# Optimization experiments

Hardware: AMD Instinct MI355X
Metric: run time of the kernel (lower is better)

The kernel has to match this reference:

```python
import jax, jax.numpy as jnp
import numpy as np

DN = ('NCHW', 'OIHW', 'NCHW')

def _conv(x, w, stride, pad, groups=1):
    return jax.lax.conv_general_dilated(x, w, (stride, stride), pad,
                                        feature_group_count=groups,
                                        dimension_numbers=DN)

def _bn(x, s, b):
    # eval-mode BatchNorm folded to per-channel affine
    return x * s[:, None, None] + b[:, None, None]

def _gelu(x):
    return jax.nn.gelu(x, approximate=False)  # torch nn.GELU default = exact erf

def _region_dw(x, dw_w, s1, b1, pw_w, s2, b2, g):
    # Vectorized RegionLayerDW: split [B,C,H,W] into g*g tiles, apply per-tile
    # depthwise3x3 -> BN -> GELU -> 1x1 -> BN -> +residual, reassemble.
    B, C, H, W = x.shape
    th, tw = H // g, W // g
    t = x.reshape(B, C, g, th, g, tw).transpose(2, 4, 0, 1, 3, 5)
    t = t.reshape(g * g, B, C, th, tw)  # [G,B,C,th,tw]
    def tile(xt, w, ts1, tb1, pw, ts2, tb2):
        h = _conv(xt, w, 1, ((1, 1), (1, 1)), groups=C)  # depthwise 3x3
        h = _gelu(_bn(h, ts1, tb1))
        h = jnp.einsum('bchw,oc->bohw', h, pw)  # 1x1 conv
        return _bn(h, ts2, tb2) + xt
    y = jax.vmap(tile)(t, dw_w, s1, b1, pw_w, s2, b2)
    y = y.reshape(g, g, B, C, th, tw).transpose(2, 3, 0, 4, 1, 5)
    return y.reshape(B, C, H, W)

def _forward(x, r1_w, r1_s, r1_b, r1_dw, r1_s1, r1_b1, r1_pw, r1_s2, r1_b2,
             r2_w, r2_s, r2_b, r2_dw, r2_s1, r2_b1, r2_pw, r2_s2, r2_b2,
             h1_w1, h1_s1, h1_b1, h1_w2, h1_s2, h1_b2, h1_w3, h1_s3, h1_b3,
             h2_w1, h2_s1, h2_b1, h2_w2, h2_s2, h2_b2,
             h3_w, h3_s, h3_b):
    B = x.shape[0]
    # region1: 5x5 conv 3->24, BN, GELU, RegionLayerDW grid 7x7; then outer GELU
    r1 = _gelu(_bn(_conv(x, r1_w, 1, ((2, 2), (2, 2))), r1_s, r1_b))
    r1 = _region_dw(r1, r1_dw, r1_s1, r1_b1, r1_pw, r1_s2, r1_b2, 7)
    region1 = _gelu(r1)
    # region2: 3x3 conv 24->48, BN, GELU, RegionLayerDW grid 4x4; outer GELU
    r2 = _gelu(_bn(_conv(region1, r2_w, 1, ((1, 1), (1, 1))), r2_s, r2_b))
    r2 = _region_dw(r2, r2_dw, r2_s1, r2_b1, r2_pw, r2_s2, r2_b2, 4)
    region2 = _gelu(r2)
    # hMLP branch1: 3 -> 48(k4s4) -> 48(k2s2) -> 256(k2s2)
    h = _gelu(_bn(_conv(x, h1_w1, 4, 'VALID'), h1_s1, h1_b1))
    h = _gelu(_bn(_conv(h, h1_w2, 2, 'VALID'), h1_s2, h1_b2))
    branch1 = _bn(_conv(h, h1_w3, 2, 'VALID'), h1_s3, h1_b3)
    # hMLP branch2: 24 -> 48(k4s4) -> 256(k4s4)
    g2 = _gelu(_bn(_conv(region1, h2_w1, 4, 'VALID'), h2_s1, h2_b1))
    branch2 = _bn(_conv(g2, h2_w2, 4, 'VALID'), h2_s2, h2_b2)
    # hMLP branch3: 48 -> 256(k16s16)
    branch3 = _bn(_conv(region2, h3_w, 16, 'VALID'), h3_s, h3_b)
    out = jnp.concatenate((branch1, branch2, branch3), axis=1)  # [B,768,14,14]
    return jnp.transpose(out.reshape(B, out.shape[1], -1), (0, 2, 1))  # [B,196,768]


def setup_inputs() -> dict:
    key = jax.random.key(0)
    ks = [key]
    def nk():
        ks[0], k = jax.random.split(ks[0])
        return k
    def rn(shape, scale=0.05):
        return jax.random.normal(nk(), shape, jnp.float32) * scale
    def sc(shape):
        return 1.0 + rn(shape)
    B = 16
    d = {}
    d['x'] = rn((B, 3, 224, 224), 1.0)
    d['r1_w'] = rn((24, 3, 5, 5)); d['r1_s'] = sc((24,)); d['r1_b'] = rn((24,))
    d['r1_dw'] = rn((49, 24, 1, 3, 3)); d['r1_s1'] = sc((49, 24)); d['r1_b1'] = rn((49, 24))
    d['r1_pw'] = rn((49, 24, 24)); d['r1_s2'] = sc((49, 24)); d['r1_b2'] = rn((49, 24))
    d['r2_w'] = rn((48, 24, 3, 3)); d['r2_s'] = sc((48,)); d['r2_b'] = rn((48,))
    d['r2_dw'] = rn((16, 48, 1, 3, 3)); d['r2_s1'] = sc((16, 48)); d['r2_b1'] = rn((16, 48))
    d['r2_pw'] = rn((16, 48, 48)); d['r2_s2'] = sc((16, 48)); d['r2_b2'] = rn((16, 48))
    d['h1_w1'] = rn((48, 3, 4, 4)); d['h1_s1'] = sc((48,)); d['h1_b1'] = rn((48,))
    d['h1_w2'] = rn((48, 48, 2, 2)); d['h1_s2'] = sc((48,)); d['h1_b2'] = rn((48,))
    d['h1_w3'] = rn((256, 48, 2, 2)); d['h1_s3'] = sc((256,)); d['h1_b3'] = rn((256,))
    d['h2_w1'] = rn((48, 24, 4, 4)); d['h2_s1'] = sc((48,)); d['h2_b1'] = rn((48,))
    d['h2_w2'] = rn((256, 48, 4, 4)); d['h2_s2'] = sc((256,)); d['h2_b2'] = rn((256,))
    d['h3_w'] = rn((256, 48, 16, 16)); d['h3_s'] = sc((256,)); d['h3_b'] = rn((256,))
    return d


def reference(x, r1_w, r1_s, r1_b, r1_dw, r1_s1, r1_b1, r1_pw, r1_s2, r1_b2,
              r2_w, r2_s, r2_b, r2_dw, r2_s1, r2_b1, r2_pw, r2_s2, r2_b2,
              h1_w1, h1_s1, h1_b1, h1_w2, h1_s2, h1_b2, h1_w3, h1_s3, h1_b3,
              h2_w1, h2_s1, h2_b1, h2_w2, h2_s2, h2_b2,
              h3_w, h3_s, h3_b):
    return _forward(x, r1_w, r1_s, r1_b, r1_dw, r1_s1, r1_b1, r1_pw, r1_s2, r1_b2,
                    r2_w, r2_s, r2_b, r2_dw, r2_s1, r2_b1, r2_pw, r2_s2, r2_b2,
                    h1_w1, h1_s1, h1_b1, h1_w2, h1_s2, h1_b2, h1_w3, h1_s3, h1_b3,
                    h2_w1, h2_s1, h2_b1, h2_w2, h2_s2, h2_b2,
                    h3_w, h3_s, h3_b)
```

## Files before the change

kernel.cpp:

```cpp
#include <hip/hip_runtime.h>
#include <hip/hip_bf16.h>
#include <math.h>

typedef __attribute__((ext_vector_type(8))) short short8;
typedef __attribute__((ext_vector_type(4))) float f32x4;

__device__ __forceinline__ float gelu_f(float x) {
  float ax = fabsf(x);
  float z = ax * 0.70710678118654752f;
  float t = __builtin_amdgcn_rcpf(1.0f + 0.3275911f * z);
  float p = t * (0.254829592f +
           t * (-0.284496736f +
           t * (1.421413741f +
           t * (-1.453152027f + t * 1.061405429f))));
  float e = __expf(-z * z);
  float erf_abs = 1.0f - p * e;
  return 0.5f * x + 0.5f * ax * erf_abs;
}

template<bool TBL, bool GELU, bool TOOUT>
__global__ __launch_bounds__(256) void convgemm_k(
    const float* __restrict__ in, const float* __restrict__ w,
    const float* __restrict__ bns, const float* __restrict__ bnb,
    float* __restrict__ out,
    int Cin, int H, int W, int ks, int stride, int pad, int ls,
    int OH, int OW, int N, int K, int ch0) {
  __shared__ __align__(16) float sA[16][64];
  __shared__ __align__(16) float sB[16][64];
  __shared__ int sTbl[256];
  const int tid = threadIdx.x;
  if (TBL) {
    int kk2 = ks * ks;
    for (int k = tid; k < K; k += 256) {
      int ic = k / kk2, r = k - ic * kk2;
      sTbl[k] = (ic << 16) | ((r / ks) << 8) | (r % ks);
    }
  }
  const int m0 = blockIdx.x * 64, n0 = blockIdx.y * 64;
  const int mm = tid >> 2, kq = tid & 3;
  const int OHW = OH * OW, HW = H * W;
  int m = m0 + mm;
  int bI = m / OHW; int r = m - bI * OHW;
  int oh = r / OW;  int ow = r - oh * OW;
  const int ihBase = oh * stride - pad, iwBase = ow * stride - pad;
  const int inBase = bI * Cin * HW;
  const int tm = tid & 15, tn = tid >> 4;
  float acc[4][4] = {};
  for (int k0 = 0; k0 < K; k0 += 16) {
    __syncthreads();
#pragma unroll
    for (int i = 0; i < 4; ++i) {
      int kk = kq * 4 + i, k = k0 + kk;
      float v = 0.0f;
      if (k < K) {
        int ic, dy, dx;
        if (TBL) {
          int tv = sTbl[k]; ic = tv >> 16; dy = (tv >> 8) & 255; dx = tv & 255;
        } else {
          ic = k >> (2 * ls);
          int r2 = k & ((1 << (2 * ls)) - 1);
          dy = r2 >> ls; dx = r2 & ((1 << ls) - 1);
        }
        int ih = ihBase + dy, iw = iwBase + dx;
        if (ih >= 0 && ih < H && iw >= 0 && iw < W)
          v = in[inBase + ic * HW + ih * W + iw];
      }
      sA[kk][mm] = v;
    }
#pragma unroll
    for (int i = 0; i < 4; ++i) {
      int kk = kq * 4 + i, k = k0 + kk;
      int n = n0 + mm;
      float v = 0.0f;
      if (n < N && k < K) v = w[n * K + k];
      sB[kk][mm] = v;
    }
    __syncthreads();
#pragma unroll
    for (int kk = 0; kk < 16; ++kk) {
      float4 a4 = *(const float4*)&sA[kk][tm * 4];
      float4 b4 = *(const float4*)&sB[kk][tn * 4];
      acc[0][0] += a4.x * b4.x; acc[0][1] += a4.x * b4.y;
      acc[0][2] += a4.x * b4.z; acc[0][3] += a4.x * b4.w;
      acc[1][0] += a4.y * b4.x; acc[1][1] += a4.y * b4.y;
      acc[1][2] += a4.y * b4.z; acc[1][3] += a4.y * b4.w;
      acc[2][0] += a4.z * b4.x; acc[2][1] += a4.z * b4.y;
      acc[2][2] += a4.z * b4.z; acc[2][3] += a4.z * b4.w;
      acc[3][0] += a4.w * b4.x; acc[3][1] += a4.w * b4.y;
      acc[3][2] += a4.w * b4.z; acc[3][3] += a4.w * b4.w;
    }
  }
#pragma unroll
  for (int i = 0; i < 4; ++i) {
    int mI = m0 + tm * 4 + i;
    int bO = mI / OHW; int rr = mI - bO * OHW;
#pragma unroll
    for (int j = 0; j < 4; ++j) {
      int n = n0 + tn * 4 + j;
      if (n < N) {
        float v = acc[i][j] * bns[n] + bnb[n];
        if (GELU) v = gelu_f(v);
        if (TOOUT) {
          out[(bO * OHW + rr) * 768 + ch0 + n] = v;
        } else {
          int oh2 = rr / OW, ow2 = rr - oh2 * OW;
          out[((bO * N + n) * OH + oh2) * OW + ow2] = v;
        }
      }
    }
  }
}

template<int CIN, int KS, int STRIDE, int PAD, int NN, int KP, bool GELU,
         int OUTMODE, int NVALID = NN>
__global__ __launch_bounds__(256) void nhwc_conv_mfma(
    const __hip_bfloat16* __restrict__ in, const __hip_bfloat16* __restrict__ wb,
    const float* __restrict__ bns, const float* __restrict__ bnb,
    float* __restrict__ out, int Hin, int Win, int OW, int OHW) {
  constexpr int K = KS * KS * CIN;
  constexpr int LROW = KP + 8;
  __shared__ __align__(16) __hip_bfloat16 sA[64][LROW];
  __shared__ __align__(16) __hip_bfloat16 sB[NN][LROW];
  const int tid = threadIdx.x;
  const float4 f4z = make_float4(0.f, 0.f, 0.f, 0.f);
  if constexpr (CIN == 4) {
    const int m = tid & 63, tg = tid >> 6;
    const int mg = blockIdx.x * 64 + m;
    const int bI = mg / OHW; int pix = mg - bI * OHW;
    const int oh = pix / OW, ow = pix - oh * OW;
    for (int dy = tg; dy < KS; dy += 4) {
      const int ih = oh * STRIDE - PAD + dy;
      __hip_bfloat16* dst = &sA[m][dy * KS * 4];
#pragma unroll
      for (int j = 0; j < KS; ++j) {
        int iw = ow * STRIDE - PAD + j;
        uint2 v = make_uint2(0u, 0u);
        if (ih >= 0 && ih < Hin && iw >= 0 && iw < Win)
          v = *(const uint2*)(in + (((size_t)bI * Hin + ih) * Win + iw) * 4);
        *(uint2*)(dst + j * 4) = v;
      }
    }
    if (tg == 3) {
      for (int c = K; c < KP; c += 4) *(uint2*)&sA[m][c] = make_uint2(0u, 0u);
    }
  } else {
    const int m = tid & 63, dy = tid >> 6;
    const int mg = blockIdx.x * 64 + m;
    const int bI = mg / OHW; int pix = mg - bI * OHW;
    const int oh = pix / OW, ow = pix - oh * OW;
    if (dy < KS) {
      const int ih = oh * STRIDE - PAD + dy;
      __hip_bfloat16* dst = &sA[m][dy * KS * CIN];
      if (ih < 0 || ih >= Hin) {
#pragma unroll
        for (int i = 0; i < KS * CIN / 8; ++i) ((float4*)dst)[i] = f4z;
      } else {
        const __hip_bfloat16* srow = in + ((size_t)bI * Hin + ih) * Win * CIN;
#pragma unroll
        for (int j = 0; j < KS; ++j) {
          int iw = ow * STRIDE - PAD + j;
          if (PAD > 0 && (iw < 0 || iw >= Win)) {
#pragma unroll
            for (int i = 0; i < CIN / 8; ++i) ((float4*)(dst + j * CIN))[i] = f4z;
          } else {
            const float4* s4 = (const float4*)(srow + (size_t)iw * CIN);
#pragma unroll
            for (int i = 0; i < CIN / 8; ++i) ((float4*)(dst + j * CIN))[i] = s4[i];
          }
        }
      }
    } else if (K < KP) {
#pragma unroll
      for (int c = K; c < KP + 8; c += 8) *(float4*)&sA[m][c] = f4z;
    }
  }
  {
    constexpr int NV = NN * KP / 8;
    const float4* w4 = (const float4*)wb;
    for (int i = tid; i < NV; i += 256) {
      int n = i / (KP / 8), c = i - n * (KP / 8);
      *(float4*)&sB[n][c * 8] = w4[i];
    }
  }
  __syncthreads();
  constexpr int NT = NN / 16;
  const int wave = tid >> 6, lane = tid & 63;
  const int fm = lane & 15, quad = lane >> 4;
  const int wm = wave * 16;
  f32x4 acc[NT] = {};
#pragma unroll
  for (int ks = 0; ks < KP / 32; ++ks) {
    short8 a = *(const short8*)&sA[wm + fm][ks * 32 + quad * 8];
#pragma unroll
    for (int j = 0; j < NT; ++j) {
      short8 b = *(const short8*)&sB[j * 16 + fm][ks * 32 + quad * 8];
      acc[j] = __builtin_amdgcn_mfma_f32_16x16x32_bf16(a, b, acc[j], 0, 0, 0);
    }
  }
  const int mg0 = blockIdx.x * 64 + wm + quad * 4;
  const int bI = mg0 / OHW, pix = mg0 - bI * OHW;
#pragma unroll
  for (int j = 0; j < NT; ++j) {
    int n = j * 16 + fm;
    if (n >= NVALID) continue;
    float s = bns[n], bb = bnb[n];
    float v[4];
#pragma unroll
    for (int e = 0; e < 4; ++e) {
      v[e] = acc[j][e] * s + bb;
      if (GELU) v[e] = gelu_f(v[e]);
    }
    if (OUTMODE == 0) {
      float4 v4 = make_float4(v[0], v[1], v[2], v[3]);
      *(float4*)&out[((size_t)(bI * NVALID + n)) * OHW + pix] = v4;
    } else {
      __hip_bfloat16* ob = (__hip_bfloat16*)out;
#pragma unroll
      for (int e = 0; e < 4; ++e)
        ob[((size_t)(bI * OHW + pix + e)) * NVALID + n] = (__hip_bfloat16)v[e];
    }
  }
}

__global__ __launch_bounds__(256, 4) void region2_mfma(
    const __hip_bfloat16* __restrict__ in, const float* __restrict__ dww,
    const float* __restrict__ s1v, const float* __restrict__ b1v,
    const __hip_bfloat16* __restrict__ pwb,
    const float* __restrict__ s2v, const float* __restrict__ b2v,
    __hip_bfloat16* __restrict__ out) {
  __shared__ __align__(16) __hip_bfloat16 sIn[10][10][56];
  __shared__ __align__(16) __hip_bfloat16 sH[64][64];
  __shared__ __align__(16) __hip_bfloat16 sW[48][64];
  __shared__ float sDW[48][9];
  __shared__ float sS1[48], sB1[48], sS2[48], sB2[48];
  const int t = blockIdx.x, sb = blockIdx.y, b = blockIdx.z;
  const int gy = t >> 2, gx = t & 3;
  const int py0 = (sb / 7) * 8, px0 = (sb % 7) * 8;
  const int Y0 = gy * 56, X0 = gx * 56;
  const int tid = threadIdx.x;
  for (int i = tid; i < 48 * 8; i += 256) {
    int n = i >> 3, g = i & 7;
    float4 v = *(const float4*)&pwb[(size_t)(t * 48 + n) * 64 + g * 8];
    *(float4*)&sW[n][((g ^ (n & 7)) * 8)] = v;
  }
  for (int i = tid; i < 432; i += 256) ((float*)sDW)[i] = dww[t * 432 + i];
  if (tid < 48) {
    sS1[tid] = s1v[t * 48 + tid]; sB1[tid] = b1v[t * 48 + tid];
    sS2[tid] = s2v[t * 48 + tid]; sB2[tid] = b2v[t * 48 + tid];
  }
  for (int i = tid; i < 600; i += 256) {
    int px = i / 6, grp = i - px * 6;
    int r = px / 10, c = px - r * 10;
    int ly = py0 + r - 1, lx = px0 + c - 1;
    uint4 v = make_uint4(0u, 0u, 0u, 0u);
    if (ly >= 0 && ly < 56 && lx >= 0 && lx < 56)
      v = *(const uint4*)(in + (((size_t)b * 224 + Y0 + ly) * 224 + X0 + lx) * 48 +
                          grp * 8);
    *(uint4*)&sIn[r][c][grp * 8] = v;
  }
  __syncthreads();
  if (tid < 192) {
    const int cg = tid >> 4;
    const int rem = tid & 15;
    const int col = rem >> 1;
    const int rh = rem & 1;
    const int ch0 = cg * 4;
    float wv[4][9], s14[4], b14[4];
#pragma unroll
    for (int c4 = 0; c4 < 4; ++c4) {
#pragma unroll
      for (int q = 0; q < 9; ++q) wv[c4][q] = sDW[ch0 + c4][q];
      s14[c4] = sS1[ch0 + c4]; b14[c4] = sB1[ch0 + c4];
    }
    float win[3][12];
#pragma unroll
    for (int rr = 0; rr < 6; ++rr) {
      int r = rh * 4 + rr;
      float* wr = win[rr % 3];
#pragma unroll
      for (int cc = 0; cc < 3; ++cc) {
        uint2 u = *(const uint2*)&sIn[r][col + cc][ch0];
        wr[cc * 4 + 0] = __uint_as_float(u.x << 16);
        wr[cc * 4 + 1] = __uint_as_float(u.x & 0xffff0000u);
        wr[cc * 4 + 2] = __uint_as_float(u.y << 16);
        wr[cc * 4 + 3] = __uint_as_float(u.y & 0xffff0000u);
      }
      if (rr >= 2) {
        const float* ra = win[(rr - 2) % 3];
        const float* rb = win[(rr - 1) % 3];
        const float* rc = win[rr % 3];
        int px = (rh * 4 + rr - 2) * 8 + col;
        __hip_bfloat16 hv[4];
#pragma unroll
        for (int c4 = 0; c4 < 4; ++c4) {
          float a = ra[c4] * wv[c4][0] + ra[4 + c4] * wv[c4][1] + ra[8 + c4] * wv[c4][2]
                  + rb[c4] * wv[c4][3] + rb[4 + c4] * wv[c4][4] + rb[8 + c4] * wv[c4][5]
                  + rc[c4] * wv[c4][6] + rc[4 + c4] * wv[c4][7] + rc[8 + c4] * wv[c4][8];
          hv[c4] = (__hip_bfloat16)gelu_f(a * s14[c4] + b14[c4]);
        }
        *(uint2*)&sH[px][((cg >> 1) ^ (px & 7)) * 8 + (cg & 1) * 4] = *(uint2*)hv;
      }
    }
  } else {
    for (int i = tid - 192; i < 128; i += 64) {
      int px = i >> 1, g = 6 + (i & 1);
      *(float4*)&sH[px][(g ^ (px & 7)) * 8] = make_float4(0.f, 0.f, 0.f, 0.f);
    }
  }
  __syncthreads();
  const int wave = tid >> 6, lane = tid & 63;
  const int fm = lane & 15, quad = lane >> 4;
  const int px = wave * 16 + fm, pxk = px & 7;
  f32x4 acc[3] = {};
#pragma unroll
  for (int ks = 0; ks < 2; ++ks) {
    short8 hb = *(const short8*)&sH[px][((ks * 4 + quad) ^ pxk) * 8];
#pragma unroll
    for (int m = 0; m < 3; ++m) {
      int wr = m * 16 + fm;
      short8 wa = *(const short8*)&sW[wr][((ks * 4 + quad) ^ (wr & 7)) * 8];
      acc[m] = __builtin_amdgcn_mfma_f32_16x16x32_bf16(wa, hb, acc[m], 0, 0, 0);
    }
  }
  const int row = px >> 3, col = px & 7;
  __hip_bfloat16* obase =
      out + (((size_t)b * 224 + Y0 + py0 + row) * 224 + X0 + px0 + col) * 48;
#pragma unroll
  for (int m = 0; m < 3; ++m) {
    int ch0m = m * 16 + quad * 4;
    uint2 ru = *(const uint2*)&sIn[row + 1][col + 1][ch0m];
    float res[4];
    res[0] = __uint_as_float(ru.x << 16);
    res[1] = __uint_as_float(ru.x & 0xffff0000u);
    res[2] = __uint_as_float(ru.y << 16);
    res[3] = __uint_as_float(ru.y & 0xffff0000u);
    __hip_bfloat16 vb[4];
#pragma unroll
    for (int e = 0; e < 4; ++e) {
      int ch = ch0m + e;
      float v = acc[m][e] * sS2[ch] + sB2[ch] + res[e];
      vb[e] = (__hip_bfloat16)gelu_f(v);
    }
    *(uint2*)&obase[ch0m] = *(uint2*)vb;
  }
}

__global__ __launch_bounds__(256, 4) void region1_mfma(
    const __hip_bfloat16* __restrict__ in, const float* __restrict__ dww,
    const float* __restrict__ s1v, const float* __restrict__ b1v,
    const __hip_bfloat16* __restrict__ pwb,
    const float* __restrict__ s2v, const float* __restrict__ b2v,
    __hip_bfloat16* __restrict__ out) {
  __shared__ __align__(16) __hip_bfloat16 sIn[10][10][24];
  __shared__ __align__(16) __hip_bfloat16 sH[64][32];
  __shared__ __align__(16) __hip_bfloat16 sW[32][32];
  __shared__ float sDW[24][9];
  __shared__ float sS1[24], sB1[24], sS2[24], sB2[24];
  const int t = blockIdx.x, sb = blockIdx.y, b = blockIdx.z;
  const int gy = t / 7, gx = t % 7;
  const int py0 = (sb >> 2) * 8, px0 = (sb & 3) * 8;
  const int Y0 = gy * 32, X0 = gx * 32;
  const int tid = threadIdx.x;
  for (int i = tid; i < 128; i += 256) {
    int n = i >> 2, g = i & 3;
    float4 v = make_float4(0.f, 0.f, 0.f, 0.f);
    if (n < 24) v = *(const float4*)&pwb[(size_t)(t * 24 + n) * 32 + g * 8];
    *(float4*)&sW[n][(g ^ (n & 3)) * 8] = v;
  }
  for (int i = tid; i < 216; i += 256) ((float*)sDW)[i] = dww[t * 216 + i];
  if (tid < 24) {
    sS1[tid] = s1v[t * 24 + tid]; sB1[tid] = b1v[t * 24 + tid];
    sS2[tid] = s2v[t * 24 + tid]; sB2[tid] = b2v[t * 24 + tid];
  }
  for (int i = tid; i < 300; i += 256) {
    int px = i / 3, grp = i - px * 3;
    int r = px / 10, c = px - r * 10;
    int ly = py0 + r - 1, lx = px0 + c - 1;
    uint4 v = make_uint4(0u, 0u, 0u, 0u);
    if (ly >= 0 && ly < 32 && lx >= 0 && lx < 32)
      v = *(const uint4*)(in + (((size_t)b * 224 + Y0 + ly) * 224 + X0 + lx) * 24 +
                          grp * 8);
    *(uint4*)&sIn[r][c][grp * 8] = v;
  }
  __syncthreads();
  if (tid < 192) {
    const int cg = tid >> 5;
    const int rem = tid & 31;
    const int col = rem >> 2;
    const int rq = rem & 3;
    const int ch0 = cg * 4;
    float wv[4][9], s14[4], b14[4];
#pragma unroll
    for (int c4 = 0; c4 < 4; ++c4) {
#pragma unroll
      for (int q = 0; q < 9; ++q) wv[c4][q] = sDW[ch0 + c4][q];
      s14[c4] = sS1[ch0 + c4]; b14[c4] = sB1[ch0 + c4];
    }
    float win[3][12];
#pragma unroll
    for (int rr = 0; rr < 4; ++rr) {
      int r = rq * 2 + rr;
      float* wr = win[rr % 3];
#pragma unroll
      for (int cc = 0; cc < 3; ++cc) {
        uint2 u = *(const uint2*)&sIn[r][col + cc][ch0];
        wr[cc * 4 + 0] = __uint_as_float(u.x << 16);
        wr[cc * 4 + 1] = __uint_as_float(u.x & 0xffff0000u);
        wr[cc * 4 + 2] = __uint_as_float(u.y << 16);
        wr[cc * 4 + 3] = __uint_as_float(u.y & 0xffff0000u);
      }
      if (rr >= 2) {
        const float* ra = win[(rr - 2) % 3];
        const float* rb = win[(rr - 1) % 3];
        const float* rc = win[rr % 3];
        int px = (rq * 2 + rr - 2) * 8 + col;
        __hip_bfloat16 hv[4];
#pragma unroll
        for (int c4 = 0; c4 < 4; ++c4) {
          float a = ra[c4] * wv[c4][0] + ra[4 + c4] * wv[c4][1] + ra[8 + c4] * wv[c4][2]
                  + rb[c4] * wv[c4][3] + rb[4 + c4] * wv[c4][4] + rb[8 + c4] * wv[c4][5]
                  + rc[c4] * wv[c4][6] + rc[4 + c4] * wv[c4][7] + rc[8 + c4] * wv[c4][8];
          hv[c4] = (__hip_bfloat16)gelu_f(a * s14[c4] + b14[c4]);
        }
        *(uint2*)&sH[px][((cg >> 1) ^ (px & 3)) * 8 + (cg & 1) * 4] = *(uint2*)hv;
      }
    }
  } else {
    int px = tid - 192;
    *(float4*)&sH[px][(3 ^ (px & 3)) * 8] = make_float4(0.f, 0.f, 0.f, 0.f);
  }
  __syncthreads();
  const int wave = tid >> 6, lane = tid & 63;
  const int fm = lane & 15, quad = lane >> 4;
  const int px = wave * 16 + fm;
  short8 hb = *(const short8*)&sH[px][(quad ^ (px & 3)) * 8];
  f32x4 acc[2] = {};
#pragma unroll
  for (int m = 0; m < 2; ++m) {
    int wr = m * 16 + fm;
    short8 wa = *(const short8*)&sW[wr][(quad ^ (wr & 3)) * 8];
    acc[m] = __builtin_amdgcn_mfma_f32_16x16x32_bf16(wa, hb, acc[m], 0, 0, 0);
  }
  const int row = px >> 3, col = px & 7;
  __hip_bfloat16* obase =
      out + (((size_t)b * 224 + Y0 + py0 + row) * 224 + X0 + px0 + col) * 24;
#pragma unroll
  for (int m = 0; m < 2; ++m) {
    int ch0m = m * 16 + quad * 4;
    if (ch0m < 24) {
      uint2 ru = *(const uint2*)&sIn[row + 1][col + 1][ch0m];
      float res[4];
      res[0] = __uint_as_float(ru.x << 16);
      res[1] = __uint_as_float(ru.x & 0xffff0000u);
      res[2] = __uint_as_float(ru.y << 16);
      res[3] = __uint_as_float(ru.y & 0xffff0000u);
      __hip_bfloat16 vb[4];
#pragma unroll
      for (int e = 0; e < 4; ++e) {
        int ch = ch0m + e;
        float v = acc[m][e] * sS2[ch] + sB2[ch] + res[e];
        vb[e] = (__hip_bfloat16)gelu_f(v);
      }
      *(uint2*)&obase[ch0m] = *(uint2*)vb;
    }
  }
}

template<int PS, int IMGW, int KTOT, int KSL, bool ATOMIC>
__global__ __launch_bounds__(256) void patch_gemm_mfma(
    const __hip_bfloat16* __restrict__ A, const __hip_bfloat16* __restrict__ Wb,
    const float* __restrict__ scale, const float* __restrict__ bias,
    float* __restrict__ out, int M, int ch0) {
  constexpr int RUN = PS * 48;
  __shared__ __align__(16) __hip_bfloat16 sA[64][64];
  __shared__ __align__(16) __hip_bfloat16 sB[64][64];
  const int tid = threadIdx.x;
  const int m0 = blockIdx.x * 64, n0 = blockIdx.y * 64;
  const int kBase = blockIdx.z * KSL;
  const int mi = tid >> 2, seg = tid & 3;
  int m = m0 + mi; int mc = (m < M) ? m : (M - 1);
  int bI = mc / 196; int r = mc - bI * 196;
  int oh = r / 14, ow = r - oh * 14;
  const __hip_bfloat16* Abase =
      A + (((size_t)bI * IMGW + oh * PS) * IMGW + ow * PS) * 48;
  const __hip_bfloat16* Wrow = Wb + (size_t)(n0 + mi) * KTOT;
  const int wave = tid >> 6, lane = tid & 63;
  const int wm = (wave & 1) * 32, wn = (wave >> 1) * 32;
  const int fm = lane & 15, quad = lane >> 4;
  const int sw = fm & 7;
  f32x4 acc[2][2] = {};
  for (int k0 = kBase; k0 < kBase + KSL; k0 += 64) {
    int dy = k0 / RUN, rem = k0 - dy * RUN;
    __syncthreads();
    {
      const __hip_bfloat16* p = Abase + (size_t)dy * IMGW * 48 + rem + seg * 16;
      float4 v0 = *(const float4*)p;
      float4 v1 = *(const float4*)(p + 8);
      int key = mi & 7;
      *(float4*)&sA[mi][((seg * 2) ^ key) * 8] = v0;
      *(float4*)&sA[mi][((seg * 2 + 1) ^ key) * 8] = v1;
      const __hip_bfloat16* q = Wrow + k0 + seg * 16;
      float4 w0 = *(const float4*)q;
      float4 w1 = *(const float4*)(q + 8);
      *(float4*)&sB[mi][((seg * 2) ^ key) * 8] = w0;
      *(float4*)&sB[mi][((seg * 2 + 1) ^ key) * 8] = w1;
    }
    __syncthreads();
#pragma unroll
    for (int ks = 0; ks < 2; ++ks) {
      int cg = (ks * 4 + quad) ^ sw;
#pragma unroll
      for (int i = 0; i < 2; ++i) {
        short8 a = *(const short8*)&sA[wm + i * 16 + fm][cg * 8];
#pragma unroll
        for (int j = 0; j < 2; ++j) {
          short8 b = *(const short8*)&sB[wn + j * 16 + fm][cg * 8];
          acc[i][j] = __builtin_amdgcn_mfma_f32_16x16x32_bf16(a, b, acc[i][j], 0, 0, 0);
        }
      }
    }
  }
#pragma unroll
  for (int i = 0; i < 2; ++i) {
#pragma unroll
    for (int j = 0; j < 2; ++j) {
      int gn = n0 + wn + j * 16 + fm;
      float sc = scale[gn];
#pragma unroll
      for (int e = 0; e < 4; ++e) {
        int gm = m0 + wm + i * 16 + quad * 4 + e;
        if (gm < M) {
          if (ATOMIC)
            atomicAdd(&out[(size_t)gm * 768 + ch0 + gn], acc[i][j][e] * sc);
          else
            out[(size_t)gm * 768 + ch0 + gn] = acc[i][j][e] * sc + bias[gn];
        }
      }
    }
  }
}

__global__ void init_b3(float* __restrict__ out, const float* __restrict__ bias) {
  int i = blockIdx.x * 256 + threadIdx.x;
  if (i < 16 * 196 * 256) {
    int n = i & 255, bp = i >> 8;
    out[bp * 768 + 512 + n] = bias[n];
  }
}

__global__ void reorder_w_k(const float* __restrict__ w, __hip_bfloat16* __restrict__ o,
                            int N, int Cin, int ks, int KP) {
  int i = blockIdx.x * 256 + threadIdx.x;
  if (i >= N * KP) return;
  int n = i / KP, k = i - n * KP;
  float v = 0.f;
  int K = ks * ks * Cin;
  if (k < K) {
    int dy = k / (ks * Cin); int r = k - dy * ks * Cin;
    int dx = r / Cin, ic = r - dx * Cin;
    v = w[((n * Cin + ic) * ks + dy) * ks + dx];
  }
  o[i] = (__hip_bfloat16)v;
}

__global__ void reorder_w4(const float* __restrict__ w, __hip_bfloat16* __restrict__ o,
                           int Nout, int Nreal, int Cp, int Cr, int ks, int KP) {
  int i = blockIdx.x * 256 + threadIdx.x;
  if (i >= Nout * KP) return;
  int n = i / KP, k = i - n * KP;
  float v = 0.f;
  if (n < Nreal && k < ks * ks * Cp) {
    int dy = k / (ks * Cp); int r = k - dy * ks * Cp;
    int dx = r / Cp, ic = r - dx * Cp;
    if (ic < Cr) v = w[((n * Cr + ic) * ks + dy) * ks + dx];
  }
  o[i] = (__hip_bfloat16)v;
}

__global__ void rw_pw(const float* __restrict__ pw, __hip_bfloat16* __restrict__ o) {
  int i = blockIdx.x * 256 + threadIdx.x;
  if (i >= 16 * 48 * 64) return;
  int t = i / 3072, r = i - t * 3072;
  int n = r >> 6, k = r & 63;
  float v = (k < 48) ? pw[(t * 48 + n) * 48 + k] : 0.f;
  o[i] = (__hip_bfloat16)v;
}

__global__ void rw_pw1(const float* __restrict__ pw, __hip_bfloat16* __restrict__ o) {
  int i = blockIdx.x * 256 + threadIdx.x;
  if (i >= 49 * 24 * 32) return;
  int t = i / 768, r = i - t * 768;
  int n = r >> 5, k = r & 31;
  float v = (k < 24) ? pw[(t * 24 + n) * 24 + k] : 0.f;
  o[i] = (__hip_bfloat16)v;
}

__global__ void xcvt(const float* __restrict__ x, __hip_bfloat16* __restrict__ o) {
  int i = blockIdx.x * 256 + threadIdx.x;
  if (i >= 802816) return;
  int b = i / 50176, p = i - b * 50176;
  const float* src = x + (size_t)b * 150528 + p;
  __hip_bfloat16 v[4];
  v[0] = (__hip_bfloat16)src[0];
  v[1] = (__hip_bfloat16)src[50176];
  v[2] = (__hip_bfloat16)src[100352];
  v[3] = (__hip_bfloat16)0.0f;
  *(uint2*)&o[(size_t)i * 4] = *(uint2*)v;
}

extern "C" void kernel_launch(void* const* d_in, const int* in_sizes, int n_in,
                              void* d_out, int out_size, void* d_ws, size_t ws_size,
                              hipStream_t stream) {
  const float* x     = (const float*)d_in[0];
  const float* r1_w  = (const float*)d_in[1];
  const float* r1_s  = (const float*)d_in[2];
  const float* r1_b  = (const float*)d_in[3];
  const float* r1_dw = (const float*)d_in[4];
  const float* r1_s1 = (const float*)d_in[5];
  const float* r1_b1 = (const float*)d_in[6];
  const float* r1_pw = (const float*)d_in[7];
  const float* r1_s2 = (const float*)d_in[8];
  const float* r1_b2 = (const float*)d_in[9];
  const float* r2_w  = (const float*)d_in[10];
  const float* r2_s  = (const float*)d_in[11];
  const float* r2_b  = (const float*)d_in[12];
  const float* r2_dw = (const float*)d_in[13];
  const float* r2_s1 = (const float*)d_in[14];
  const float* r2_b1 = (const float*)d_in[15];
  const float* r2_pw = (const float*)d_in[16];
  const float* r2_s2 = (const float*)d_in[17];
  const float* r2_b2 = (const float*)d_in[18];
  const float* h1_w1 = (const float*)d_in[19];
  const float* h1_s1 = (const float*)d_in[20];
  const float* h1_b1 = (const float*)d_in[21];
  const float* h1_w2 = (const float*)d_in[22];
  const float* h1_s2 = (const float*)d_in[23];
  const float* h1_b2 = (const float*)d_in[24];
  const float* h1_w3 = (const float*)d_in[25];
  const float* h1_s3 = (const float*)d_in[26];
  const float* h1_b3 = (const float*)d_in[27];
  const float* h2_w1 = (const float*)d_in[28];
  const float* h2_s1 = (const float*)d_in[29];
  const float* h2_b1 = (const float*)d_in[30];
  const float* h2_w2 = (const float*)d_in[31];
  const float* h2_s2 = (const float*)d_in[32];
  const float* h2_b2 = (const float*)d_in[33];
  const float* h3_w  = (const float*)d_in[34];
  const float* h3_s  = (const float*)d_in[35];
  const float* h3_b  = (const float*)d_in[36];
  float* out = (float*)d_out;

  float* F = (float*)d_ws;
  __hip_bfloat16* R1b   = (__hip_bfloat16*)F;
  __hip_bfloat16* C5b   = (__hip_bfloat16*)(F + 9633792);
  __hip_bfloat16* T1b   = (__hip_bfloat16*)(F + 9633792);
  __hip_bfloat16* T2b   = (__hip_bfloat16*)(F + 28901376);
  __hip_bfloat16* h3wb  = (__hip_bfloat16*)(F + 48168960);
  __hip_bfloat16* r2wb  = (__hip_bfloat16*)(F + 49741824);
  __hip_bfloat16* h2w1b = (__hip_bfloat16*)(F + 49747200);
  __hip_bfloat16* pw2wb = (__hip_bfloat16*)(F + 49756416);
  __hip_bfloat16* r1wb  = (__hip_bfloat16*)(F + 49780992);
  __hip_bfloat16* h2w2b = (__hip_bfloat16*)(F + 49783040);
  __hip_bfloat16* xb    = (__hip_bfloat16*)(F + 49881344);
  __hip_bfloat16* S1b   = (__hip_bfloat16*)(F + 51486976);
  float* S1             = F + 52691200;
  float* S2             = F + 55099648;
  __hip_bfloat16* pw1wb = (__hip_bfloat16*)(F + 55701760);

  dim3 blk(256);

  xcvt<<<dim3(3136), blk, 0, stream>>>(x, xb);
  reorder_w_k<<<dim3(12288), blk, 0, stream>>>(h3_w, h3wb, 256, 48, 16, 12288);
  reorder_w_k<<<dim3(42), blk, 0, stream>>>(r2_w, r2wb, 48, 24, 3, 224);
  reorder_w_k<<<dim3(72), blk, 0, stream>>>(h2_w1, h2w1b, 48, 24, 4, 384);
  reorder_w_k<<<dim3(768), blk, 0, stream>>>(h2_w2, h2w2b, 256, 48, 4, 768);
  reorder_w4<<<dim3(16), blk, 0, stream>>>(r1_w, r1wb, 32, 24, 4, 3, 5, 128);
  rw_pw<<<dim3(192), blk, 0, stream>>>(r2_pw, pw2wb);
  rw_pw1<<<dim3(147), blk, 0, stream>>>(r1_pw, pw1wb);

  nhwc_conv_mfma<4, 5, 1, 2, 32, 128, true, 1, 24><<<dim3(12544), blk, 0, stream>>>(
      xb, r1wb, r1_s, r1_b, (float*)C5b, 224, 224, 224, 50176);
  region1_mfma<<<dim3(49, 16, 16), blk, 0, stream>>>(
      C5b, r1_dw, r1_s1, r1_b1, pw1wb, r1_s2, r1_b2, R1b);
  nhwc_conv_mfma<24, 4, 4, 0, 48, 384, true, 1><<<dim3(784), blk, 0, stream>>>(
      R1b, h2w1b, h2_s1, h2_b1, (float*)S1b, 224, 224, 56, 3136);
  patch_gemm_mfma<4, 56, 768, 768, false><<<dim3(49, 4, 1), blk, 0, stream>>>(
      S1b, h2w2b, h2_s2, h2_b2, out, 3136, 256);
  convgemm_k<false, true, false><<<dim3(784, 1), blk, 0, stream>>>(
      x, h1_w1, h1_s1, h1_b1, S1, 3, 224, 224, 4, 4, 0, 2, 56, 56, 48, 48, 0);
  convgemm_k<false, true, false><<<dim3(196, 1), blk, 0, stream>>>(
      S1, h1_w2, h1_s2, h1_b2, S2, 48, 56, 56, 2, 2, 0, 1, 28, 28, 48, 192, 0);
  convgemm_k<false, false, true><<<dim3(49, 4), blk, 0, stream>>>(
      S2, h1_w3, h1_s3, h1_b3, out, 48, 28, 28, 2, 2, 0, 1, 14, 14, 256, 192, 0);
  init_b3<<<dim3(3136), blk, 0, stream>>>(out, h3_b);
  nhwc_conv_mfma<24, 3, 1, 1, 48, 224, true, 1><<<dim3(12544), blk, 0, stream>>>(
      R1b, r2wb, r2_s, r2_b, (float*)T1b, 224, 224, 224, 50176);
  region2_mfma<<<dim3(16, 49, 16), blk, 0, stream>>>(
      T1b, r2_dw, r2_s1, r2_b1, pw2wb, r2_s2, r2_b2, T2b);
  patch_gemm_mfma<16, 224, 12288, 1536, true><<<dim3(49, 4, 8), blk, 0, stream>>>(
      T2b, h3wb, h3_s, h3_b, out, 3136, 512);
  (void)in_sizes; (void)n_in; (void)out_size; (void)ws_size;
}
```

Before: 571.3 us.

## Add halo-tiled MFMA kernel for region2 3x3 conv with LDS input reuse

Replaces the generic NHWC implicit-GEMM conv for the 24->48 3x3 conv with a dedicated kernel. Each block covers an 8x32 output tile and stages a 10x34 halo of the input plus all weights in LDS. The MFMA fragments are then read straight from the halo rows, so no im2col gather is needed. This is meant to cut redundant global loads of the input, at the cost of more LDS use per block and a layout tied to this shape.

```diff
diff --git a/kernel.cpp b/kernel.cpp
--- a/kernel.cpp
+++ b/kernel.cpp
@@ -218,6 +218,80 @@
 #pragma unroll
       for (int e = 0; e < 4; ++e)
         ob[((size_t)(bI * OHW + pix + e)) * NVALID + n] = (__hip_bfloat16)v[e];
+    }
+  }
+}
+
+__global__ __launch_bounds__(256, 4) void conv3_tile_mfma(
+    const __hip_bfloat16* __restrict__ in,
+    const __hip_bfloat16* __restrict__ wb,
+    const float* __restrict__ bns, const float* __restrict__ bnb,
+    __hip_bfloat16* __restrict__ out) {
+  __shared__ __align__(16) __hip_bfloat16 sIn[11][816];
+  __shared__ __align__(16) __hip_bfloat16 sB[48][232];
+  __shared__ float sS[48], sBb[48];
+  const int tid = threadIdx.x;
+  const int X0 = blockIdx.x * 32, Y0 = blockIdx.y * 8, b = blockIdx.z;
+  {
+    const float4* w4 = (const float4*)wb;
+    for (int i = tid; i < 1344; i += 256) {
+      int n = i / 28, c = i - n * 28;
+      *(float4*)&sB[n][c * 8] = w4[i];
+    }
+  }
+  if (tid < 48) { sS[tid] = bns[tid]; sBb[tid] = bnb[tid]; }
+  for (int i = tid; i < 1020; i += 256) {
+    int r = i / 102, c8 = i - r * 102;
+    int p = c8 / 3;
+    int iy = Y0 - 1 + r, ix = X0 - 1 + p;
+    uint4 v = make_uint4(0u, 0u, 0u, 0u);
+    if (iy >= 0 && iy < 224 && ix >= 0 && ix < 224)
+      v = *(const uint4*)(in + (((size_t)b * 224 + iy) * 224 + ix) * 24 +
+                          (c8 - p * 3) * 8);
+    *(uint4*)&sIn[r][c8 * 8] = v;
+  }
+  for (int i = tid; i < 102; i += 256)
+    *(uint4*)&sIn[10][i * 8] = make_uint4(0u, 0u, 0u, 0u);
+  __syncthreads();
+  const int wave = tid >> 6, lane = tid & 63;
+  const int fm = lane & 15, quad = lane >> 4;
+  f32x4 acc[4][3] = {};
+#pragma unroll
+  for (int ks = 0; ks < 7; ++ks) {
+    const int k0 = ks * 32 + quad * 8;
+    const int dy = k0 / 72;
+    const int u = k0 - dy * 72;
+    short8 wfr[3];
+#pragma unroll
+    for (int cg = 0; cg < 3; ++cg)
+      wfr[cg] = *(const short8*)&sB[cg * 16 + fm][k0];
+#pragma unroll
+    for (int pg = 0; pg < 4; ++pg) {
+      const int r = 2 * wave + (pg >> 1);
+      const int c = (pg & 1) * 16 + fm;
+      short8 pf = *(const short8*)&sIn[r + dy][c * 24 + u];
+#pragma unroll
+      for (int cg = 0; cg < 3; ++cg)
+        acc[pg][cg] = __builtin_amdgcn_mfma_f32_16x16x32_bf16(
+            wfr[cg], pf, acc[pg][cg], 0, 0, 0);
+    }
+  }
+#pragma unroll
+  for (int pg = 0; pg < 4; ++pg) {
+    const int row = Y0 + 2 * wave + (pg >> 1);
+    const int col = X0 + (pg & 1) * 16 + fm;
+    __hip_bfloat16* obase = out + (((size_t)b * 224 + row) * 224 + col) * 48;
+#pragma unroll
+    for (int cg = 0; cg < 3; ++cg) {
+      const int ch0 = cg * 16 + quad * 4;
+      __hip_bfloat16 vb[4];
+#pragma unroll
+      for (int e = 0; e < 4; ++e) {
+        const int ch = ch0 + e;
+        float v = acc[pg][cg][e] * sS[ch] + sBb[ch];
+        vb[e] = (__hip_bfloat16)gelu_f(v);
+      }
+      *(uint2*)&obase[ch0] = *(uint2*)vb;
     }
   }
 }
@@ -693,8 +767,8 @@
   convgemm_k<false, false, true><<<dim3(49, 4), blk, 0, stream>>>(
       S2, h1_w3, h1_s3, h1_b3, out, 48, 28, 28, 2, 2, 0, 1, 14, 14, 256, 192, 0);
   init_b3<<<dim3(3136), blk, 0, stream>>>(out, h3_b);
-  nhwc_conv_mfma<24, 3, 1, 1, 48, 224, true, 1><<<dim3(12544), blk, 0, stream>>>(
-      R1b, r2wb, r2_s, r2_b, (float*)T1b, 224, 224, 224, 50176);
+  conv3_tile_mfma<<<dim3(7, 28, 16), blk, 0, stream>>>(
+      R1b, r2wb, r2_s, r2_b, T1b);
   region2_mfma<<<dim3(16, 49, 16), blk, 0, stream>>>(
       T1b, r2_dw, r2_s1, r2_b1, pw2wb, r2_s2, r2_b2, T2b);
   patch_gemm_mfma<16, 224, 12288, 1536, true><<<dim3(49, 4, 8), blk, 0, stream>>>(
```

After: 537.1 us. -6.0%, faster.

## Fuse region2 3x3 conv into region2 depthwise/pointwise kernel

Applied to the files above, without the earlier changes.

Computes the 24->48 3x3 conv with BN+GELU inside the region2 kernel via MFMA on a 12x12 halo tile loaded into shared memory, instead of writing the 48-channel bf16 T1 intermediate to global memory and reading it back. This removes one kernel launch and a large intermediate round trip. In exchange it recomputes the conv on the 10x10 halo for each 8x8 output tile (about 56% redundant conv work), reloads the conv weights per block, and aliases shared memory across phases.

```diff
diff --git a/kernel.cpp b/kernel.cpp
--- a/kernel.cpp
+++ b/kernel.cpp
@@ -222,22 +222,79 @@
   }
 }
 
-__global__ __launch_bounds__(256, 4) void region2_mfma(
-    const __hip_bfloat16* __restrict__ in, const float* __restrict__ dww,
+__global__ __launch_bounds__(256, 4) void c3r2_fused(
+    const __hip_bfloat16* __restrict__ in,
+    const __hip_bfloat16* __restrict__ wc3,
+    const float* __restrict__ c3s, const float* __restrict__ c3b,
+    const float* __restrict__ dww,
     const float* __restrict__ s1v, const float* __restrict__ b1v,
     const __hip_bfloat16* __restrict__ pwb,
     const float* __restrict__ s2v, const float* __restrict__ b2v,
     __hip_bfloat16* __restrict__ out) {
-  __shared__ __align__(16) __hip_bfloat16 sIn[10][10][56];
-  __shared__ __align__(16) __hip_bfloat16 sH[64][64];
-  __shared__ __align__(16) __hip_bfloat16 sW[48][64];
-  __shared__ float sDW[48][9];
-  __shared__ float sS1[48], sB1[48], sS2[48], sB2[48];
+  __shared__ __align__(16) __hip_bfloat16 sC3[10][10][56];
+  __shared__ __align__(16) unsigned char uS[29760];
+  __hip_bfloat16 (*sWc3)[232] = (__hip_bfloat16(*)[232])uS;
+  __hip_bfloat16* sIn12 = (__hip_bfloat16*)(uS + 22272);
+  __hip_bfloat16 (*sH)[64] = (__hip_bfloat16(*)[64])uS;
+  __hip_bfloat16 (*sW)[64] = (__hip_bfloat16(*)[64])(uS + 8192);
+  float (*sDW)[9] = (float(*)[9])(uS + 14336);
+  float* sS1 = (float*)(uS + 16064);
+  float* sB1 = sS1 + 48; float* sS2 = sB1 + 48; float* sB2 = sS2 + 48;
+
   const int t = blockIdx.x, sb = blockIdx.y, b = blockIdx.z;
   const int gy = t >> 2, gx = t & 3;
   const int py0 = (sb / 7) * 8, px0 = (sb % 7) * 8;
   const int Y0 = gy * 56, X0 = gx * 56;
   const int tid = threadIdx.x;
+
+  {
+    const float4* w4 = (const float4*)wc3;
+    for (int i = tid; i < 1344; i += 256) {
+      int n = i / 28, c = i - n * 28;
+      *(float4*)&sWc3[n][c * 8] = w4[i];
+    }
+  }
+  for (int i = tid; i < 468; i += 256) {
+    int r = i / 36, rem = i - r * 36;
+    int p = rem / 3, g = rem - p * 3;
+    int iy = Y0 + py0 - 2 + r, ix = X0 + px0 - 2 + p;
+    uint4 v = make_uint4(0u, 0u, 0u, 0u);
+    if (r < 12 && iy >= 0 && iy < 224 && ix >= 0 && ix < 224)
+      v = *(const uint4*)(in + (((size_t)b * 224 + iy) * 224 + ix) * 24 + g * 8);
+    *(uint4*)&sIn12[r * 288 + p * 24 + g * 8] = v;
+  }
+  __syncthreads();
+  const int wave = tid >> 6, lane = tid & 63;
+  const int fm = lane & 15, quad = lane >> 4;
+  int rcOff[2], pP[2];
+#pragma unroll
+  for (int pgi = 0; pgi < 2; ++pgi) {
+    int p = (wave * 2 + pgi) * 16 + fm;
+    pP[pgi] = p;
+    int pv = p < 100 ? p : 99;
+    int r = pv / 10, c = pv - r * 10;
+    rcOff[pgi] = r * 288 + c * 24;
+  }
+  f32x4 c3acc[2][3] = {};
+#pragma unroll
+  for (int ks = 0; ks < 7; ++ks) {
+    const int k0 = ks * 32 + quad * 8;
+    const int dy = k0 / 72;
+    const int u = k0 - dy * 72;
+    short8 wfr[3];
+#pragma unroll
+    for (int cg = 0; cg < 3; ++cg)
+      wfr[cg] = *(const short8*)&sWc3[cg * 16 + fm][k0];
+#pragma unroll
+    for (int pgi = 0; pgi < 2; ++pgi) {
+      short8 pf = *(const short8*)&sIn12[rcOff[pgi] + dy * 288 + u];
+#pragma unroll
+      for (int cg = 0; cg < 3; ++cg)
+        c3acc[pgi][cg] = __builtin_amdgcn_mfma_f32_16x16x32_bf16(
+            wfr[cg], pf, c3acc[pgi][cg], 0, 0, 0);
+    }
+  }
+  __syncthreads();
   for (int i = tid; i < 48 * 8; i += 256) {
     int n = i >> 3, g = i & 7;
     float4 v = *(const float4*)&pwb[(size_t)(t * 48 + n) * 64 + g * 8];
@@ -248,15 +305,30 @@
     sS1[tid] = s1v[t * 48 + tid]; sB1[tid] = b1v[t * 48 + tid];
     sS2[tid] = s2v[t * 48 + tid]; sB2[tid] = b2v[t * 48 + tid];
   }
-  for (int i = tid; i < 600; i += 256) {
-    int px = i / 6, grp = i - px * 6;
-    int r = px / 10, c = px - r * 10;
-    int ly = py0 + r - 1, lx = px0 + c - 1;
-    uint4 v = make_uint4(0u, 0u, 0u, 0u);
-    if (ly >= 0 && ly < 56 && lx >= 0 && lx < 56)
-      v = *(const uint4*)(in + (((size_t)b * 224 + Y0 + ly) * 224 + X0 + lx) * 48 +
-                          grp * 8);
-    *(uint4*)&sIn[r][c][grp * 8] = v;
+#pragma unroll
+  for (int pgi = 0; pgi < 2; ++pgi) {
+    int p = pP[pgi];
+    if (p < 100) {
+      int r = p / 10, c = p - (p / 10) * 10;
+      int ty = py0 - 1 + r, tx = px0 - 1 + c;
+      bool valid = (ty >= 0) && (ty < 56) && (tx >= 0) && (tx < 56);
+#pragma unroll
+      for (int cg = 0; cg < 3; ++cg) {
+        int ch0 = cg * 16 + quad * 4;
+        float4 sc = *(const float4*)&c3s[ch0];
+        float4 bi = *(const float4*)&c3b[ch0];
+        float vv[4];
+        vv[0] = c3acc[pgi][cg][0] * sc.x + bi.x;
+        vv[1] = c3acc[pgi][cg][1] * sc.y + bi.y;
+        vv[2] = c3acc[pgi][cg][2] * sc.z + bi.z;
+        vv[3] = c3acc[pgi][cg][3] * sc.w + bi.w;
+        __hip_bfloat16 vb[4];
+#pragma unroll
+        for (int e = 0; e < 4; ++e)
+          vb[e] = (__hip_bfloat16)(valid ? gelu_f(vv[e]) : 0.0f);
+        *(uint2*)&sC3[r][c][ch0] = *(uint2*)vb;
+      }
+    }
   }
   __syncthreads();
   if (tid < 192) {
@@ -279,7 +351,7 @@
       float* wr = win[rr % 3];
 #pragma unroll
       for (int cc = 0; cc < 3; ++cc) {
-        uint2 u = *(const uint2*)&sIn[r][col + cc][ch0];
+        uint2 u = *(const uint2*)&sC3[r][col + cc][ch0];
         wr[cc * 4 + 0] = __uint_as_float(u.x << 16);
         wr[cc * 4 + 1] = __uint_as_float(u.x & 0xffff0000u);
         wr[cc * 4 + 2] = __uint_as_float(u.y << 16);
@@ -308,40 +380,40 @@
     }
   }
   __syncthreads();
-  const int wave = tid >> 6, lane = tid & 63;
-  const int fm = lane & 15, quad = lane >> 4;
-  const int px = wave * 16 + fm, pxk = px & 7;
-  f32x4 acc[3] = {};
-#pragma unroll
-  for (int ks = 0; ks < 2; ++ks) {
-    short8 hb = *(const short8*)&sH[px][((ks * 4 + quad) ^ pxk) * 8];
+  {
+    const int px = wave * 16 + fm, pxk = px & 7;
+    f32x4 acc[3] = {};
+#pragma unroll
+    for (int ks = 0; ks < 2; ++ks) {
+      short8 hb = *(const short8*)&sH[px][((ks * 4 + quad) ^ pxk) * 8];
+#pragma unroll
+      for (int m = 0; m < 3; ++m) {
+        int wr = m * 16 + fm;
+        short8 wa = *(const short8*)&sW[wr][((ks * 4 + quad) ^ (wr & 7)) * 8];
+        acc[m] = __builtin_amdgcn_mfma_f32_16x16x32_bf16(wa, hb, acc[m], 0, 0, 0);
+      }
+    }
+    const int row = px >> 3, col = px & 7;
+    __hip_bfloat16* obase =
+        out + (((size_t)b * 224 + Y0 + py0 + row) * 224 + X0 + px0 + col) * 48;
 #pragma unroll
     for (int m = 0; m < 3; ++m) {
-      int wr = m * 16 + fm;
-      short8 wa = *(const short8*)&sW[wr][((ks * 4 + quad) ^ (wr & 7)) * 8];
-      acc[m] = __builtin_amdgcn_mfma_f32_16x16x32_bf16(wa, hb, acc[m], 0, 0, 0);
-    }
-  }
-  const int row = px >> 3, col = px & 7;
-  __hip_bfloat16* obase =
-      out + (((size_t)b * 224 + Y0 + py0 + row) * 224 + X0 + px0 + col) * 48;
-#pragma unroll
-  for (int m = 0; m < 3; ++m) {
-    int ch0m = m * 16 + quad * 4;
-    uint2 ru = *(const uint2*)&sIn[row + 1][col + 1][ch0m];
-    float res[4];
-    res[0] = __uint_as_float(ru.x << 16);
-    res[1] = __uint_as_float(ru.x & 0xffff0000u);
-    res[2] = __uint_as_float(ru.y << 16);
-    res[3] = __uint_as_float(ru.y & 0xffff0000u);
-    __hip_bfloat16 vb[4];
-#pragma unroll
-    for (int e = 0; e < 4; ++e) {
-      int ch = ch0m + e;
-      float v = acc[m][e] * sS2[ch] + sB2[ch] + res[e];
-      vb[e] = (__hip_bfloat16)gelu_f(v);
-    }
-    *(uint2*)&obase[ch0m] = *(uint2*)vb;
+      int ch0m = m * 16 + quad * 4;
+      uint2 ru = *(const uint2*)&sC3[row + 1][col + 1][ch0m];
+      float res[4];
+      res[0] = __uint_as_float(ru.x << 16);
+      res[1] = __uint_as_float(ru.x & 0xffff0000u);
+      res[2] = __uint_as_float(ru.y << 16);
+      res[3] = __uint_as_float(ru.y & 0xffff0000u);
+      __hip_bfloat16 vb[4];
+#pragma unroll
+      for (int e = 0; e < 4; ++e) {
+        int ch = ch0m + e;
+        float v = acc[m][e] * sS2[ch] + sB2[ch] + res[e];
+        vb[e] = (__hip_bfloat16)gelu_f(v);
+      }
+      *(uint2*)&obase[ch0m] = *(uint2*)vb;
+    }
   }
 }
 
@@ -653,7 +725,6 @@
   float* F = (float*)d_ws;
   __hip_bfloat16* R1b   = (__hip_bfloat16*)F;
   __hip_bfloat16* C5b   = (__hip_bfloat16*)(F + 9633792);
-  __hip_bfloat16* T1b   = (__hip_bfloat16*)(F + 9633792);
   __hip_bfloat16* T2b   = (__hip_bfloat16*)(F + 28901376);
   __hip_bfloat16* h3wb  = (__hip_bfloat16*)(F + 48168960);
   __hip_bfloat16* r2wb  = (__hip_bfloat16*)(F + 49741824);
@@ -693,10 +764,8 @@
   convgemm_k<false, false, true><<<dim3(49, 4), blk, 0, stream>>>(
       S2, h1_w3, h1_s3, h1_b3, out, 48, 28, 28, 2, 2, 0, 1, 14, 14, 256, 192, 0);
   init_b3<<<dim3(3136), blk, 0, stream>>>(out, h3_b);
-  nhwc_conv_mfma<24, 3, 1, 1, 48, 224, true, 1><<<dim3(12544), blk, 0, stream>>>(
-      R1b, r2wb, r2_s, r2_b, (float*)T1b, 224, 224, 224, 50176);
-  region2_mfma<<<dim3(16, 49, 16), blk, 0, stream>>>(
-      T1b, r2_dw, r2_s1, r2_b1, pw2wb, r2_s2, r2_b2, T2b);
+  c3r2_fused<<<dim3(16, 49, 16), blk, 0, stream>>>(
+      R1b, r2wb, r2_s, r2_b, r2_dw, r2_s1, r2_b1, pw2wb, r2_s2, r2_b2, T2b);
   patch_gemm_mfma<16, 224, 12288, 1536, true><<<dim3(49, 4, 8), blk, 0, stream>>>(
       T2b, h3wb, h3_s, h3_b, out, 3136, 512);
   (void)in_sizes; (void)n_in; (void)out_size; (void)ws_size;
```

Result: no change. 566.2 us (-0.9%).
